# Optimization experiments

Hardware: AMD Instinct MI355X
Metric: run time of the kernel (lower is better)

The kernel has to match this reference:

```python
import jax, jax.numpy as jnp
import numpy as np

B, H, W, C = 4, 64, 64, 128
NH, K = 4, 7
HD = C // NH
MLPD = 4 * C
EPS = 1e-5

def _ln(x, g, b):
    m = x.mean(-1, keepdims=True)
    v = ((x - m) ** 2).mean(-1, keepdims=True)
    return (x - m) * jax.lax.rsqrt(v + EPS) * g + b

def setup_inputs() -> dict:
    key = jax.random.key(0)
    ks = jax.random.split(key, 10)
    rn = lambda k, s: jax.random.normal(k, s, dtype=jnp.float32) * 0.02
    return {
        'query': jax.random.normal(ks[0], (B, H, W, C), dtype=jnp.float32),
        'key_value': jax.random.normal(ks[1], (B, H, W, C), dtype=jnp.float32),
        'g1': jnp.ones((C,), jnp.float32), 'b1': jnp.zeros((C,), jnp.float32),
        'g2': jnp.ones((C,), jnp.float32), 'b2': jnp.zeros((C,), jnp.float32),
        'g3': jnp.ones((C,), jnp.float32), 'b3': jnp.zeros((C,), jnp.float32),
        'Wq': rn(ks[2], (C, C)), 'bq': jnp.zeros((C,), jnp.float32),
        'Wkv': rn(ks[3], (C, 2 * C)), 'bkv': jnp.zeros((2 * C,), jnp.float32),
        'Wp': rn(ks[4], (C, C)), 'bp': jnp.zeros((C,), jnp.float32),
        'rpb': rn(ks[5], (NH, 2 * K - 1, 2 * K - 1)),
        'W1': rn(ks[6], (C, MLPD)), 'bm1': jnp.zeros((MLPD,), jnp.float32),
        'W2': rn(ks[7], (MLPD, C)), 'bm2': jnp.zeros((C,), jnp.float32),
    }

def _nat(qn, kvn, Wq, bq, Wkv, bkv, Wp, bp, rpb):
    # NATTEN-style 2D neighborhood attention (clamped KxK window at borders)
    q = (qn @ Wq + bq).reshape(B, H, W, NH, HD) * (HD ** -0.5)
    kv = (kvn @ Wkv + bkv).reshape(B, H, W, 2, NH, HD)
    k, v = kv[..., 0, :, :], kv[..., 1, :, :]
    ii = jnp.clip(jnp.arange(H) - K // 2, 0, H - K)[:, None] + jnp.arange(K)  # [H,K]
    jj = jnp.clip(jnp.arange(W) - K // 2, 0, W - K)[:, None] + jnp.arange(K)  # [W,K]
    def gather(t):  # [B,H,W,NH,HD] -> [B,H,W,NH,K*K,HD]
        t = jnp.take(t, ii, axis=1)   # [B,H,K,W,NH,HD]
        t = jnp.take(t, jj, axis=3)   # [B,H,K,W,K,NH,HD]
        return t.transpose(0, 1, 3, 5, 2, 4, 6).reshape(B, H, W, NH, K * K, HD)
    kn, vn = gather(k), gather(v)
    scores = jnp.einsum('bijhd,bijhnd->bijhn', q, kn)  # [B,H,W,NH,K*K]
    # relative positional bias: offsets in [-(K-1), K-1] -> index into 2K-1 table
    ri = ii - jnp.arange(H)[:, None] + (K - 1)  # [H,K]
    rj = jj - jnp.arange(W)[:, None] + (K - 1)  # [W,K]
    bias = rpb[:, ri]                   # [NH,H,K,2K-1]
    bias = jnp.take(bias, rj, axis=3)   # [NH,H,K,W,K]
    bias = bias.transpose(1, 3, 0, 2, 4).reshape(H, W, NH, K * K)
    attn = jax.nn.softmax(scores + bias[None], axis=-1)
    out = jnp.einsum('bijhn,bijhnd->bijhd', attn, vn).reshape(B, H, W, C)
    return out @ Wp + bp

def reference(query, key_value, g1, b1, g2, b2, g3, b3, Wq, bq, Wkv, bkv, Wp, bp, rpb, W1, bm1, W2, bm2):
    shortcut = key_value
    qn = _ln(query, g1, b1)
    kvn = _ln(key_value, g2, b2)
    x = shortcut + _nat(qn, kvn, Wq, bq, Wkv, bkv, Wp, bp, rpb)
    h = _ln(x, g3, b3)
    h = jax.nn.gelu(h @ W1 + bm1, approximate=False) @ W2 + bm2
    return x + h
```

## Files before the change

kernel.cpp:

```cpp
#include <hip/hip_runtime.h>
#include <math.h>

#define TOK 16384

typedef __attribute__((ext_vector_type(8))) __bf16 bf16x8;
typedef __attribute__((ext_vector_type(4))) float f32x4;

__device__ inline unsigned short f2bf(float f) {
    union { float f; unsigned int u; } v; v.f = f;
    unsigned int r = v.u + 0x7fffu + ((v.u >> 16) & 1u);
    return (unsigned short)(r >> 16);
}
__device__ inline float gelu_exact(float v) {
    return 0.5f * v * (1.0f + erff(v * 0.70710678118654752f));
}

__global__ __launch_bounds__(256) void wtrans_kernel(
    const float* __restrict__ Wq, const float* __restrict__ Wkv,
    const float* __restrict__ Wp, const float* __restrict__ W1, const float* __restrict__ W2,
    unsigned short* __restrict__ Wt)
{
    __shared__ float tile[32][33];
    int t = blockIdx.x, tid = threadIdx.x;
    const float* src; unsigned short* dst; int Kd, Nd, li;
    if      (t < 16)  { src = Wq;  dst = Wt;          Kd = 128; Nd = 128; li = t; }
    else if (t < 48)  { src = Wkv; dst = Wt + 16384;  Kd = 128; Nd = 256; li = t - 16; }
    else if (t < 64)  { src = Wp;  dst = Wt + 49152;  Kd = 128; Nd = 128; li = t - 48; }
    else if (t < 128) { src = W1;  dst = Wt + 65536;  Kd = 128; Nd = 512; li = t - 64; }
    else              { src = W2;  dst = Wt + 131072; Kd = 512; Nd = 128; li = t - 128; }
    int ntc = Nd >> 5;
    int k0 = (li / ntc) * 32, n0 = (li % ntc) * 32;
    int r = tid >> 3, c4 = (tid & 7) * 4;
    float4 v = *(const float4*)(src + (size_t)(k0 + r) * Nd + n0 + c4);
    tile[r][c4 + 0] = v.x; tile[r][c4 + 1] = v.y;
    tile[r][c4 + 2] = v.z; tile[r][c4 + 3] = v.w;
    __syncthreads();
    ushort4 o;
    o.x = f2bf(tile[c4 + 0][r]);
    o.y = f2bf(tile[c4 + 1][r]);
    o.z = f2bf(tile[c4 + 2][r]);
    o.w = f2bf(tile[c4 + 3][r]);
    *(ushort4*)(dst + (size_t)(n0 + r) * Kd + k0 + c4) = o;
}

__global__ __launch_bounds__(256) void qkvln_kernel(
    const float* __restrict__ query, const float* __restrict__ key_value,
    const float* __restrict__ g1, const float* __restrict__ b1,
    const float* __restrict__ g2, const float* __restrict__ b2,
    const unsigned short* __restrict__ Wt,
    const float* __restrict__ bq, const float* __restrict__ bkv,
    unsigned short* __restrict__ qbh, unsigned short* __restrict__ kbh,
    unsigned short* __restrict__ vbh, float qscale)
{
    __shared__ __align__(16) unsigned short aq[16 * 136];
    __shared__ __align__(16) unsigned short akv[16 * 136];
    const int tid = threadIdx.x;
    const int wave = tid >> 6, lane = tid & 63;
    const int lr = lane & 15, lg = lane >> 4;
    const int m0 = blockIdx.x * 16;

    {
        const int r = tid >> 4, t16 = tid & 15;
#pragma unroll
        for (int which = 0; which < 2; ++which) {
            const float* xr = (which ? key_value : query) + (size_t)(m0 + r) * 128 + t16 * 8;
            float4 v0 = *(const float4*)xr;
            float4 v1 = *(const float4*)(xr + 4);
            float s = v0.x + v0.y + v0.z + v0.w + v1.x + v1.y + v1.z + v1.w;
            s += __shfl_xor(s, 1); s += __shfl_xor(s, 2);
            s += __shfl_xor(s, 4); s += __shfl_xor(s, 8);
            float mean = s * (1.0f / 128.0f);
            float d0 = v0.x - mean, d1 = v0.y - mean, d2 = v0.z - mean, d3 = v0.w - mean;
            float d4 = v1.x - mean, d5 = v1.y - mean, d6 = v1.z - mean, d7 = v1.w - mean;
            float vv = d0*d0 + d1*d1 + d2*d2 + d3*d3 + d4*d4 + d5*d5 + d6*d6 + d7*d7;
            vv += __shfl_xor(vv, 1); vv += __shfl_xor(vv, 2);
            vv += __shfl_xor(vv, 4); vv += __shfl_xor(vv, 8);
            float rs = rsqrtf(vv * (1.0f / 128.0f) + 1e-5f);
            const float* g = which ? g2 : g1;
            const float* bb = which ? b2 : b1;
            float4 ga = *(const float4*)(g + t16 * 8);
            float4 gb = *(const float4*)(g + t16 * 8 + 4);
            float4 ba = *(const float4*)(bb + t16 * 8);
            float4 bbb = *(const float4*)(bb + t16 * 8 + 4);
            ushort4 oa, ob;
            oa.x = f2bf(d0 * rs * ga.x + ba.x); oa.y = f2bf(d1 * rs * ga.y + ba.y);
            oa.z = f2bf(d2 * rs * ga.z + ba.z); oa.w = f2bf(d3 * rs * ga.w + ba.w);
            ob.x = f2bf(d4 * rs * gb.x + bbb.x); ob.y = f2bf(d5 * rs * gb.y + bbb.y);
            ob.z = f2bf(d6 * rs * gb.z + bbb.z); ob.w = f2bf(d7 * rs * gb.w + bbb.w);
            unsigned short* dst = (which ? akv : aq) + r * 136 + t16 * 8;
            *(ushort4*)dst = oa;
            *(ushort4*)(dst + 4) = ob;
        }
    }
    __syncthreads();

#pragma unroll
    for (int t = 0; t < 6; ++t) {
        int j = wave + 4 * t;
        const unsigned short* A = (j < 8) ? aq : akv;
        const unsigned short* Wb = (j < 8) ? (Wt + (size_t)(j * 16 + lr) * 128)
                                           : (Wt + 16384 + (size_t)((j - 8) * 16 + lr) * 128);
        f32x4 acc = {0.f, 0.f, 0.f, 0.f};
#pragma unroll
        for (int kk = 0; kk < 4; ++kk) {
            bf16x8 af = *(const bf16x8*)&A[lr * 136 + kk * 32 + lg * 8];
            bf16x8 wf = *(const bf16x8*)(Wb + kk * 32 + lg * 8);
            acc = __builtin_amdgcn_mfma_f32_16x16x32_bf16(af, wf, acc, 0, 0, 0);
        }
        if (j < 8) {
            int gc = j * 16 + lr;
            float bs = bq[gc];
#pragma unroll
            for (int r = 0; r < 4; ++r)
                qbh[(size_t)(m0 + lg * 4 + r) * 128 + gc] = f2bf((acc[r] + bs) * qscale);
        } else {
            int gc = (j - 8) * 16 + lr;
            float bs = bkv[gc];
            if (gc < 128) {
#pragma unroll
                for (int r = 0; r < 4; ++r)
                    kbh[(size_t)(m0 + lg * 4 + r) * 128 + gc] = f2bf(acc[r] + bs);
            } else {
#pragma unroll
                for (int r = 0; r < 4; ++r)
                    vbh[(size_t)(m0 + lg * 4 + r) * 128 + gc - 128] = f2bf(acc[r] + bs);
            }
        }
    }
}

__global__ __launch_bounds__(256, 4) void nat_attn(
    const unsigned short* __restrict__ qbh,
    const unsigned short* __restrict__ kbh,
    const unsigned short* __restrict__ vbh,
    const float* __restrict__ rpb,
    unsigned short* __restrict__ out)
{
    __shared__ __align__(16) unsigned short shm[16384];
    unsigned short* kS = shm;
    unsigned short* vT = shm + 8960;
    unsigned short* Pb = shm;
    float* rpbs = (float*)(shm + 4608);
    const int tid = threadIdx.x;
    const int wave = tid >> 6, lane = tid & 63;
    const int lr = lane & 15, lg = lane >> 4;
    const int bid = blockIdx.x;
    const int tile = bid & 63, h = (bid >> 6) & 3, b = bid >> 8;
    const int ti0 = (tile >> 3) * 8, tj0 = (tile & 7) * 8;
    const int hr0 = min(max(ti0 - 3, 0), 50);
    const int hc0 = min(max(tj0 - 3, 0), 50);
    const int bb = b << 12;

    for (int u = tid; u < 896; u += 256) {
        int tok = u >> 2, chunk = u & 3;
        int tr = tok >> 4, tc = tok & 15;
        size_t src = (size_t)(bb + (hr0 + tr) * 64 + hc0 + tc) * 128 + h * 32 + chunk * 8;
        int4 kw = *(const int4*)(kbh + src);
        *(int4*)&kS[tok * 40 + chunk * 8] = kw;
        int4 vw = *(const int4*)(vbh + src);
        const unsigned short* v8 = (const unsigned short*)&vw;
#pragma unroll
        for (int k = 0; k < 8; ++k)
            vT[(chunk * 8 + k) * 232 + tok] = v8[k];
    }

    const int gi_m = ti0 + wave * 2 + (lr >> 3);
    const int gj_m = tj0 + (lr & 7);
    const int tq = bb + gi_m * 64 + gj_m;
    bf16x8 qf = *(const bf16x8*)(qbh + (size_t)tq * 128 + h * 32 + lg * 8);
    __syncthreads();

    f32x4 S[14];
#pragma unroll
    for (int kb = 0; kb < 14; ++kb) {
        bf16x8 kf = *(const bf16x8*)&kS[(kb * 16 + lr) * 40 + lg * 8];
        f32x4 z = {0.f, 0.f, 0.f, 0.f};
        S[kb] = __builtin_amdgcn_mfma_f32_16x16x32_bf16(qf, kf, z, 0, 0, 0);
    }
    __syncthreads();

    if (tid < 169) rpbs[tid] = rpb[h * 169 + tid];
    __syncthreads();

#pragma unroll
    for (int i = 0; i < 4; ++i) {
        int m = lg * 4 + i;
        int gi = ti0 + wave * 2 + (m >> 3);
        int gj = tj0 + (m & 7);
        int si = min(max(gi - 3, 0), 57), sj = min(max(gj - 3, 0), 57);
        bool cv = (unsigned)(hc0 + lr - sj) < 7u;
        int rjc = min(max(hc0 + lr - gj + 6, 0), 12);
        float mxi = -INFINITY;
#pragma unroll
        for (int kb = 0; kb < 14; ++kb) {
            bool rv = (unsigned)(hr0 + kb - si) < 7u;
            int ric = min(max(hr0 + kb - gi + 6, 0), 12);
            float bias = rpbs[rjc + ric * 13];
            float s = (rv && cv) ? S[kb][i] + bias : -1e30f;
            S[kb][i] = s;
            mxi = fmaxf(mxi, s);
        }
        mxi = fmaxf(mxi, __shfl_xor(mxi, 1));
        mxi = fmaxf(mxi, __shfl_xor(mxi, 2));
        mxi = fmaxf(mxi, __shfl_xor(mxi, 4));
        mxi = fmaxf(mxi, __shfl_xor(mxi, 8));
        float smi = 0.0f;
#pragma unroll
        for (int kb = 0; kb < 14; ++kb) {
            float e = __expf(S[kb][i] - mxi);
            S[kb][i] = e;
            smi += e;
        }
        smi += __shfl_xor(smi, 1);
        smi += __shfl_xor(smi, 2);
        smi += __shfl_xor(smi, 4);
        smi += __shfl_xor(smi, 8);
        float rinv = 1.0f / smi;
#pragma unroll
        for (int kb = 0; kb < 14; ++kb) S[kb][i] *= rinv;
    }

    f32x4 O[2] = {};
#pragma unroll
    for (int r = 0; r < 4; ++r) {
        const int nk = (r < 3) ? 4 : 2;
#pragma unroll
        for (int i = 0; i < 4; ++i) {
            int m = lg * 4 + i;
#pragma unroll
            for (int kbl = 0; kbl < 4; ++kbl) {
                if (kbl < nk)
                    Pb[(wave * 16 + m) * 72 + kbl * 16 + lr] = f2bf(S[r * 4 + kbl][i]);
            }
        }
#pragma unroll
        for (int ksl = 0; ksl < 2; ++ksl) {
            if (ksl * 2 < nk) {
                bf16x8 pf = *(const bf16x8*)&Pb[(wave * 16 + lr) * 72 + ksl * 32 + lg * 8];
#pragma unroll
                for (int nb = 0; nb < 2; ++nb) {
                    bf16x8 vf = *(const bf16x8*)&vT[(nb * 16 + lr) * 232 + r * 64 + ksl * 32 + lg * 8];
                    O[nb] = __builtin_amdgcn_mfma_f32_16x16x32_bf16(pf, vf, O[nb], 0, 0, 0);
                }
            }
        }
    }

#pragma unroll
    for (int i = 0; i < 4; ++i) {
        int m = lg * 4 + i;
        int gi = ti0 + wave * 2 + (m >> 3);
        int gj = tj0 + (m & 7);
        size_t t = ((size_t)(bb + gi * 64 + gj)) * 128 + h * 32;
        out[t + lr]      = f2bf(O[0][i]);
        out[t + 16 + lr] = f2bf(O[1][i]);
    }
}

__global__ __launch_bounds__(256) void tail_kernel(
    const unsigned short* __restrict__ attnh,
    const unsigned short* __restrict__ WtP,
    const unsigned short* __restrict__ W1t,
    const unsigned short* __restrict__ W2t,
    const float* __restrict__ bp, const float* __restrict__ bm1, const float* __restrict__ bm2,
    const float* __restrict__ resk,
    const float* __restrict__ g3, const float* __restrict__ b3,
    float* __restrict__ dout)
{
    __shared__ float xs[16][132];
    __shared__ __align__(16) unsigned short xnS[16 * 136];
    __shared__ __align__(16) unsigned short hS[16 * 520];
    const int tid = threadIdx.x;
    const int wave = tid >> 6, lane = tid & 63;
    const int lr = lane & 15, lg = lane >> 4;
    const int m0 = blockIdx.x * 16;

#pragma unroll
    for (int t = 0; t < 2; ++t) {
        int colt = wave + 4 * t;
        int tok = m0 + lr;
        f32x4 acc = {0.f, 0.f, 0.f, 0.f};
#pragma unroll
        for (int kk = 0; kk < 4; ++kk) {
            bf16x8 af = *(const bf16x8*)(attnh + (size_t)tok * 128 + kk * 32 + lg * 8);
            bf16x8 wf = *(const bf16x8*)(WtP + (size_t)(colt * 16 + lr) * 128 + kk * 32 + lg * 8);
            acc = __builtin_amdgcn_mfma_f32_16x16x32_bf16(af, wf, acc, 0, 0, 0);
        }
        int gc = colt * 16 + lr;
        float bs = bp[gc];
#pragma unroll
        for (int r = 0; r < 4; ++r) {
            int row = lg * 4 + r;
            xs[row][gc] = acc[r] + bs + resk[(size_t)(m0 + row) * 128 + gc];
        }
    }
    __syncthreads();

    {
        const int r = tid >> 4, t16 = tid & 15;
        float vals[8];
#pragma unroll
        for (int jj = 0; jj < 8; ++jj) vals[jj] = xs[r][t16 * 8 + jj];
        float s = 0.0f;
#pragma unroll
        for (int jj = 0; jj < 8; ++jj) s += vals[jj];
        s += __shfl_xor(s, 1); s += __shfl_xor(s, 2);
        s += __shfl_xor(s, 4); s += __shfl_xor(s, 8);
        float mean = s * (1.0f / 128.0f);
        float vv = 0.0f;
#pragma unroll
        for (int jj = 0; jj < 8; ++jj) { float d = vals[jj] - mean; vv += d * d; }
        vv += __shfl_xor(vv, 1); vv += __shfl_xor(vv, 2);
        vv += __shfl_xor(vv, 4); vv += __shfl_xor(vv, 8);
        float rs = rsqrtf(vv * (1.0f / 128.0f) + 1e-5f);
        float4 ga = *(const float4*)(g3 + t16 * 8);
        float4 gb = *(const float4*)(g3 + t16 * 8 + 4);
        float4 ba = *(const float4*)(b3 + t16 * 8);
        float4 bbv = *(const float4*)(b3 + t16 * 8 + 4);
        ushort4 oa, ob;
        oa.x = f2bf((vals[0] - mean) * rs * ga.x + ba.x);
        oa.y = f2bf((vals[1] - mean) * rs * ga.y + ba.y);
        oa.z = f2bf((vals[2] - mean) * rs * ga.z + ba.z);
        oa.w = f2bf((vals[3] - mean) * rs * ga.w + ba.w);
        ob.x = f2bf((vals[4] - mean) * rs * gb.x + bbv.x);
        ob.y = f2bf((vals[5] - mean) * rs * gb.y + bbv.y);
        ob.z = f2bf((vals[6] - mean) * rs * gb.z + bbv.z);
        ob.w = f2bf((vals[7] - mean) * rs * gb.w + bbv.w);
        *(ushort4*)&xnS[r * 136 + t16 * 8] = oa;
        *(ushort4*)&xnS[r * 136 + t16 * 8 + 4] = ob;
    }
    __syncthreads();

#pragma unroll
    for (int t = 0; t < 8; ++t) {
        int colt = wave + 4 * t;
        f32x4 acc = {0.f, 0.f, 0.f, 0.f};
#pragma unroll
        for (int kk = 0; kk < 4; ++kk) {
            bf16x8 wf = *(const bf16x8*)(W1t + (size_t)(colt * 16 + lr) * 128 + kk * 32 + lg * 8);
            bf16x8 xf = *(const bf16x8*)&xnS[lr * 136 + kk * 32 + lg * 8];
            acc = __builtin_amdgcn_mfma_f32_16x16x32_bf16(wf, xf, acc, 0, 0, 0);
        }
        int chb = colt * 16 + lg * 4;
        float4 bs = *(const float4*)(bm1 + chb);
        ushort4 pk;
        pk.x = f2bf(gelu_exact(acc[0] + bs.x));
        pk.y = f2bf(gelu_exact(acc[1] + bs.y));
        pk.z = f2bf(gelu_exact(acc[2] + bs.z));
        pk.w = f2bf(gelu_exact(acc[3] + bs.w));
        *(ushort4*)&hS[lr * 520 + chb] = pk;
    }
    __syncthreads();

#pragma unroll
    for (int t = 0; t < 2; ++t) {
        int colt = wave + 4 * t;
        f32x4 acc = {0.f, 0.f, 0.f, 0.f};
#pragma unroll
        for (int kk = 0; kk < 16; ++kk) {
            bf16x8 hf = *(const bf16x8*)&hS[lr * 520 + kk * 32 + lg * 8];
            bf16x8 wf = *(const bf16x8*)(W2t + (size_t)(colt * 16 + lr) * 512 + kk * 32 + lg * 8);
            acc = __builtin_amdgcn_mfma_f32_16x16x32_bf16(hf, wf, acc, 0, 0, 0);
        }
        int gc = colt * 16 + lr;
        float bs = bm2[gc];
#pragma unroll
        for (int r = 0; r < 4; ++r) {
            int row = lg * 4 + r;
            dout[(size_t)(m0 + row) * 128 + gc] = acc[r] + bs + xs[row][gc];
        }
    }
}

extern "C" void kernel_launch(void* const* d_in, const int* in_sizes, int n_in,
                              void* d_out, int out_size, void* d_ws, size_t ws_size,
                              hipStream_t stream) {
    const float* query     = (const float*)d_in[0];
    const float* key_value = (const float*)d_in[1];
    const float* g1 = (const float*)d_in[2];
    const float* b1 = (const float*)d_in[3];
    const float* g2 = (const float*)d_in[4];
    const float* b2 = (const float*)d_in[5];
    const float* g3 = (const float*)d_in[6];
    const float* b3 = (const float*)d_in[7];
    const float* Wq  = (const float*)d_in[8];
    const float* bq  = (const float*)d_in[9];
    const float* Wkv = (const float*)d_in[10];
    const float* bkv = (const float*)d_in[11];
    const float* Wp  = (const float*)d_in[12];
    const float* bp  = (const float*)d_in[13];
    const float* rpb = (const float*)d_in[14];
    const float* W1  = (const float*)d_in[15];
    const float* bm1 = (const float*)d_in[16];
    const float* W2  = (const float*)d_in[17];
    const float* bm2 = (const float*)d_in[18];

    char* ws = (char*)d_ws;
    unsigned short* qbh   = (unsigned short*)(ws + 0);
    unsigned short* kbh   = (unsigned short*)(ws + 4194304);
    unsigned short* vbh   = (unsigned short*)(ws + 8388608);
    unsigned short* attnh = (unsigned short*)(ws + 12582912);
    unsigned short* Wt    = (unsigned short*)(ws + 16777216);

    const float qscale = 0.17677669529663687f;

    wtrans_kernel<<<192, 256, 0, stream>>>(Wq, Wkv, Wp, W1, W2, Wt);
    qkvln_kernel<<<1024, 256, 0, stream>>>(query, key_value, g1, b1, g2, b2,
                                           Wt, bq, bkv, qbh, kbh, vbh, qscale);
    nat_attn<<<1024, 256, 0, stream>>>(qbh, kbh, vbh, rpb, attnh);
    tail_kernel<<<1024, 256, 0, stream>>>(attnh, Wt + 49152, Wt + 65536, Wt + 131072,
                                          bp, bm1, bm2, key_value, g3, b3, (float*)d_out);
}
```

Measured before the change: 167.8 us.

## Fuse all four stages into one cooperative kernel with grid-wide barriers

Turns the weight transpose, LN+QKV projection, neighborhood attention and MLP tail into device functions and runs them in one persistent cooperative kernel of 1024 blocks, separated by grid.sync(). The goal is to remove the launch gaps and tail drains between four separate launches. If the cooperative launch fails (for example because 1024 blocks cannot all be resident), it falls back to the original four-kernel sequence. Costs include grid-barrier latency, all stages sharing one 32KB shared-memory buffer, and register pressure fixed by the heaviest stage at 4 blocks per CU.

```diff
diff --git a/kernel.cpp b/kernel.cpp
--- a/kernel.cpp
+++ b/kernel.cpp
@@ -1,5 +1,8 @@
 #include <hip/hip_runtime.h>
+#include <hip/hip_cooperative_groups.h>
 #include <math.h>
+
+namespace cg = cooperative_groups;
 
 #define TOK 16384
 
@@ -15,13 +18,12 @@
     return 0.5f * v * (1.0f + erff(v * 0.70710678118654752f));
 }
 
-__global__ __launch_bounds__(256) void wtrans_kernel(
+
+__device__ __forceinline__ void wtrans_body(
     const float* __restrict__ Wq, const float* __restrict__ Wkv,
     const float* __restrict__ Wp, const float* __restrict__ W1, const float* __restrict__ W2,
-    unsigned short* __restrict__ Wt)
-{
-    __shared__ float tile[32][33];
-    int t = blockIdx.x, tid = threadIdx.x;
+    unsigned short* __restrict__ Wt, float* tile , int t, int tid)
+{
     const float* src; unsigned short* dst; int Kd, Nd, li;
     if      (t < 16)  { src = Wq;  dst = Wt;          Kd = 128; Nd = 128; li = t; }
     else if (t < 48)  { src = Wkv; dst = Wt + 16384;  Kd = 128; Nd = 256; li = t - 16; }
@@ -32,33 +34,30 @@
     int k0 = (li / ntc) * 32, n0 = (li % ntc) * 32;
     int r = tid >> 3, c4 = (tid & 7) * 4;
     float4 v = *(const float4*)(src + (size_t)(k0 + r) * Nd + n0 + c4);
-    tile[r][c4 + 0] = v.x; tile[r][c4 + 1] = v.y;
-    tile[r][c4 + 2] = v.z; tile[r][c4 + 3] = v.w;
+    tile[r * 33 + c4 + 0] = v.x; tile[r * 33 + c4 + 1] = v.y;
+    tile[r * 33 + c4 + 2] = v.z; tile[r * 33 + c4 + 3] = v.w;
     __syncthreads();
     ushort4 o;
-    o.x = f2bf(tile[c4 + 0][r]);
-    o.y = f2bf(tile[c4 + 1][r]);
-    o.z = f2bf(tile[c4 + 2][r]);
-    o.w = f2bf(tile[c4 + 3][r]);
+    o.x = f2bf(tile[(c4 + 0) * 33 + r]);
+    o.y = f2bf(tile[(c4 + 1) * 33 + r]);
+    o.z = f2bf(tile[(c4 + 2) * 33 + r]);
+    o.w = f2bf(tile[(c4 + 3) * 33 + r]);
     *(ushort4*)(dst + (size_t)(n0 + r) * Kd + k0 + c4) = o;
 }
 
-__global__ __launch_bounds__(256) void qkvln_kernel(
+__device__ __forceinline__ void qkvln_body(
     const float* __restrict__ query, const float* __restrict__ key_value,
     const float* __restrict__ g1, const float* __restrict__ b1,
     const float* __restrict__ g2, const float* __restrict__ b2,
     const unsigned short* __restrict__ Wt,
     const float* __restrict__ bq, const float* __restrict__ bkv,
     unsigned short* __restrict__ qbh, unsigned short* __restrict__ kbh,
-    unsigned short* __restrict__ vbh, float qscale)
-{
-    __shared__ __align__(16) unsigned short aq[16 * 136];
-    __shared__ __align__(16) unsigned short akv[16 * 136];
-    const int tid = threadIdx.x;
+    unsigned short* __restrict__ vbh, float qscale,
+    unsigned short* aq , unsigned short* akv , int bid, int tid)
+{
     const int wave = tid >> 6, lane = tid & 63;
     const int lr = lane & 15, lg = lane >> 4;
-    const int m0 = blockIdx.x * 16;
-
+    const int m0 = bid * 16;
     {
         const int r = tid >> 4, t16 = tid & 15;
 #pragma unroll
@@ -93,7 +92,6 @@
         }
     }
     __syncthreads();
-
 #pragma unroll
     for (int t = 0; t < 6; ++t) {
         int j = wave + 4 * t;
@@ -129,22 +127,18 @@
     }
 }
 
-__global__ __launch_bounds__(256, 4) void nat_attn(
-    const unsigned short* __restrict__ qbh,
-    const unsigned short* __restrict__ kbh,
-    const unsigned short* __restrict__ vbh,
-    const float* __restrict__ rpb,
-    unsigned short* __restrict__ out)
-{
-    __shared__ __align__(16) unsigned short shm[16384];
+__device__ __forceinline__ void attn_body(
+    const unsigned short* __restrict__ qbh, const unsigned short* __restrict__ kbh,
+    const unsigned short* __restrict__ vbh, const float* __restrict__ rpb,
+    unsigned short* __restrict__ out, unsigned short* shm ,
+    int bid, int tid)
+{
     unsigned short* kS = shm;
     unsigned short* vT = shm + 8960;
     unsigned short* Pb = shm;
     float* rpbs = (float*)(shm + 4608);
-    const int tid = threadIdx.x;
     const int wave = tid >> 6, lane = tid & 63;
     const int lr = lane & 15, lg = lane >> 4;
-    const int bid = blockIdx.x;
     const int tile = bid & 63, h = (bid >> 6) & 3, b = bid >> 8;
     const int ti0 = (tile >> 3) * 8, tj0 = (tile & 7) * 8;
     const int hr0 = min(max(ti0 - 3, 0), 50);
@@ -163,7 +157,6 @@
         for (int k = 0; k < 8; ++k)
             vT[(chunk * 8 + k) * 232 + tok] = v8[k];
     }
-
     const int gi_m = ti0 + wave * 2 + (lr >> 3);
     const int gj_m = tj0 + (lr & 7);
     const int tq = bb + gi_m * 64 + gj_m;
@@ -245,7 +238,6 @@
             }
         }
     }
-
 #pragma unroll
     for (int i = 0; i < 4; ++i) {
         int m = lg * 4 + i;
@@ -257,23 +249,20 @@
     }
 }
 
-__global__ __launch_bounds__(256) void tail_kernel(
+__device__ __forceinline__ void tail_body(
     const unsigned short* __restrict__ attnh,
-    const unsigned short* __restrict__ WtP,
-    const unsigned short* __restrict__ W1t,
+    const unsigned short* __restrict__ WtP, const unsigned short* __restrict__ W1t,
     const unsigned short* __restrict__ W2t,
     const float* __restrict__ bp, const float* __restrict__ bm1, const float* __restrict__ bm2,
-    const float* __restrict__ resk,
-    const float* __restrict__ g3, const float* __restrict__ b3,
-    float* __restrict__ dout)
-{
-    __shared__ float xs[16][132];
-    __shared__ __align__(16) unsigned short xnS[16 * 136];
-    __shared__ __align__(16) unsigned short hS[16 * 520];
-    const int tid = threadIdx.x;
+    const float* __restrict__ resk, const float* __restrict__ g3, const float* __restrict__ b3,
+    float* __restrict__ dout, unsigned char* smem, int bid, int tid)
+{
+    float* xs = (float*)smem;
+    unsigned short* xnS = (unsigned short*)(smem + 8448);
+    unsigned short* hS  = (unsigned short*)(smem + 12800);
     const int wave = tid >> 6, lane = tid & 63;
     const int lr = lane & 15, lg = lane >> 4;
-    const int m0 = blockIdx.x * 16;
+    const int m0 = bid * 16;
 
 #pragma unroll
     for (int t = 0; t < 2; ++t) {
@@ -291,16 +280,15 @@
 #pragma unroll
         for (int r = 0; r < 4; ++r) {
             int row = lg * 4 + r;
-            xs[row][gc] = acc[r] + bs + resk[(size_t)(m0 + row) * 128 + gc];
-        }
-    }
-    __syncthreads();
-
+            xs[row * 132 + gc] = acc[r] + bs + resk[(size_t)(m0 + row) * 128 + gc];
+        }
+    }
+    __syncthreads();
     {
         const int r = tid >> 4, t16 = tid & 15;
         float vals[8];
 #pragma unroll
-        for (int jj = 0; jj < 8; ++jj) vals[jj] = xs[r][t16 * 8 + jj];
+        for (int jj = 0; jj < 8; ++jj) vals[jj] = xs[r * 132 + t16 * 8 + jj];
         float s = 0.0f;
 #pragma unroll
         for (int jj = 0; jj < 8; ++jj) s += vals[jj];
@@ -330,7 +318,6 @@
         *(ushort4*)&xnS[r * 136 + t16 * 8 + 4] = ob;
     }
     __syncthreads();
-
 #pragma unroll
     for (int t = 0; t < 8; ++t) {
         int colt = wave + 4 * t;
@@ -351,7 +338,6 @@
         *(ushort4*)&hS[lr * 520 + chb] = pk;
     }
     __syncthreads();
-
 #pragma unroll
     for (int t = 0; t < 2; ++t) {
         int colt = wave + 4 * t;
@@ -367,9 +353,70 @@
 #pragma unroll
         for (int r = 0; r < 4; ++r) {
             int row = lg * 4 + r;
-            dout[(size_t)(m0 + row) * 128 + gc] = acc[r] + bs + xs[row][gc];
-        }
-    }
+            dout[(size_t)(m0 + row) * 128 + gc] = acc[r] + bs + xs[row * 132 + gc];
+        }
+    }
+}
+
+struct KParams {
+    const float *query, *key_value, *g1, *b1, *g2, *b2, *g3, *b3;
+    const float *Wq, *bq, *Wkv, *bkv, *Wp, *bp, *rpb, *W1, *bm1, *W2, *bm2;
+    unsigned short *qbh, *kbh, *vbh, *attnh, *Wt;
+    float *dout;
+    float qscale;
+};
+
+__global__ __launch_bounds__(256, 4) void fused_kernel(KParams p)
+{
+    __shared__ __align__(16) unsigned char smem[32768];
+    cg::grid_group grid = cg::this_grid();
+    const int tid = threadIdx.x, bid = blockIdx.x;
+
+    if (bid < 192)
+        wtrans_body(p.Wq, p.Wkv, p.Wp, p.W1, p.W2, p.Wt, (float*)smem, bid, tid);
+    grid.sync();
+    qkvln_body(p.query, p.key_value, p.g1, p.b1, p.g2, p.b2, p.Wt, p.bq, p.bkv,
+               p.qbh, p.kbh, p.vbh, p.qscale,
+               (unsigned short*)smem, (unsigned short*)smem + 2176, bid, tid);
+    grid.sync();
+    attn_body(p.qbh, p.kbh, p.vbh, p.rpb, p.attnh, (unsigned short*)smem, bid, tid);
+    grid.sync();
+    tail_body(p.attnh, p.Wt + 49152, p.Wt + 65536, p.Wt + 131072,
+              p.bp, p.bm1, p.bm2, p.key_value, p.g3, p.b3, p.dout, smem, bid, tid);
+}
+
+__global__ __launch_bounds__(256) void wtrans_kernel(
+    const float* Wq, const float* Wkv, const float* Wp, const float* W1, const float* W2,
+    unsigned short* Wt)
+{
+    __shared__ float tile[32 * 33];
+    wtrans_body(Wq, Wkv, Wp, W1, W2, Wt, tile, blockIdx.x, threadIdx.x);
+}
+__global__ __launch_bounds__(256) void qkvln_kernel(
+    const float* query, const float* key_value,
+    const float* g1, const float* b1, const float* g2, const float* b2,
+    const unsigned short* Wt, const float* bq, const float* bkv,
+    unsigned short* qbh, unsigned short* kbh, unsigned short* vbh, float qscale)
+{
+    __shared__ __align__(16) unsigned short s[4352];
+    qkvln_body(query, key_value, g1, b1, g2, b2, Wt, bq, bkv, qbh, kbh, vbh, qscale,
+               s, s + 2176, blockIdx.x, threadIdx.x);
+}
+__global__ __launch_bounds__(256, 4) void nat_attn(
+    const unsigned short* qbh, const unsigned short* kbh, const unsigned short* vbh,
+    const float* rpb, unsigned short* out)
+{
+    __shared__ __align__(16) unsigned short shm[16384];
+    attn_body(qbh, kbh, vbh, rpb, out, shm, blockIdx.x, threadIdx.x);
+}
+__global__ __launch_bounds__(256) void tail_kernel(
+    const unsigned short* attnh, const unsigned short* WtP, const unsigned short* W1t,
+    const unsigned short* W2t, const float* bp, const float* bm1, const float* bm2,
+    const float* resk, const float* g3, const float* b3, float* dout)
+{
+    __shared__ __align__(16) unsigned char smem[29440];
+    tail_body(attnh, WtP, W1t, W2t, bp, bm1, bm2, resk, g3, b3, dout,
+              smem, blockIdx.x, threadIdx.x);
 }
 
 extern "C" void kernel_launch(void* const* d_in, const int* in_sizes, int n_in,
@@ -404,10 +451,23 @@
 
     const float qscale = 0.17677669529663687f;
 
-    wtrans_kernel<<<192, 256, 0, stream>>>(Wq, Wkv, Wp, W1, W2, Wt);
-    qkvln_kernel<<<1024, 256, 0, stream>>>(query, key_value, g1, b1, g2, b2,
-                                           Wt, bq, bkv, qbh, kbh, vbh, qscale);
-    nat_attn<<<1024, 256, 0, stream>>>(qbh, kbh, vbh, rpb, attnh);
-    tail_kernel<<<1024, 256, 0, stream>>>(attnh, Wt + 49152, Wt + 65536, Wt + 131072,
-                                          bp, bm1, bm2, key_value, g3, b3, (float*)d_out);
-}
+    KParams p;
+    p.query = query; p.key_value = key_value;
+    p.g1 = g1; p.b1 = b1; p.g2 = g2; p.b2 = b2; p.g3 = g3; p.b3 = b3;
+    p.Wq = Wq; p.bq = bq; p.Wkv = Wkv; p.bkv = bkv; p.Wp = Wp; p.bp = bp;
+    p.rpb = rpb; p.W1 = W1; p.bm1 = bm1; p.W2 = W2; p.bm2 = bm2;
+    p.qbh = qbh; p.kbh = kbh; p.vbh = vbh; p.attnh = attnh; p.Wt = Wt;
+    p.dout = (float*)d_out; p.qscale = qscale;
+
+    void* args[] = { (void*)&p };
+    hipError_t err = hipLaunchCooperativeKernel((const void*)fused_kernel,
+                                                dim3(1024), dim3(256), args, 0, stream);
+    if (err != hipSuccess) {
+        wtrans_kernel<<<192, 256, 0, stream>>>(Wq, Wkv, Wp, W1, W2, Wt);
+        qkvln_kernel<<<1024, 256, 0, stream>>>(query, key_value, g1, b1, g2, b2,
+                                               Wt, bq, bkv, qbh, kbh, vbh, qscale);
+        nat_attn<<<1024, 256, 0, stream>>>(qbh, kbh, vbh, rpb, attnh);
+        tail_kernel<<<1024, 256, 0, stream>>>(attnh, Wt + 49152, Wt + 65536, Wt + 131072,
+                                              bp, bm1, bm2, key_value, g3, b3, (float*)d_out);
+    }
+}
```

Result: slower. 538.1 us (+220.7%).
